# Optimization experiments

Hardware: AMD Instinct MI355X
Metric: run time of the kernel (lower is better)

Reference implementation:

```python
import jax, jax.numpy as jnp
import numpy as np

HEADS = 8
DIM_HEAD = 64
MAX_REL = 200  # max_rel_dist


def setup_inputs() -> dict:
    key = jax.random.key(0)
    ks = jax.random.split(key, 5)
    B, N, D = 4, 2048, 512
    x = jax.random.normal(ks[0], (B, N, D), dtype=jnp.float32)
    temporal_mask = jax.random.randint(ks[1], (N, N), 0, 2, dtype=jnp.int32)
    gamma = jnp.ones((D,), jnp.float32)
    beta = jnp.zeros((D,), jnp.float32)
    Wqkv = jax.random.normal(ks[2], (D, 3 * HEADS * DIM_HEAD), dtype=jnp.float32) * 0.02
    Wout = jax.random.normal(ks[3], (HEADS * DIM_HEAD, D), dtype=jnp.float32) * 0.02
    bout = jnp.zeros((D,), jnp.float32)
    rel_table = jax.random.normal(ks[4], (2 * MAX_REL - 1,), dtype=jnp.float32) * 0.02
    return {"x": x, "gamma": gamma, "beta": beta, "Wqkv": Wqkv, "Wout": Wout,
            "bout": bout, "rel_table": rel_table, "temporal_mask": temporal_mask}


def reference(x, gamma, beta, Wqkv, Wout, bout, rel_table, temporal_mask):
    B, N, D = x.shape
    scale = DIM_HEAD ** -0.5
    # LayerNorm
    mu = jnp.mean(x, axis=-1, keepdims=True)
    var = jnp.mean(jnp.square(x - mu), axis=-1, keepdims=True)
    xn = (x - mu) * jax.lax.rsqrt(var + 1e-5) * gamma + beta
    # QKV projection (no bias), split heads: b n (h d) -> b h n d
    qkv = xn @ Wqkv  # [B, N, 3*H*d]
    q, k, v = jnp.split(qkv, 3, axis=-1)
    split = lambda t: t.reshape(B, N, HEADS, DIM_HEAD).transpose(0, 2, 1, 3)
    q, k, v = split(q), split(k), split(v)
    # scores with learned relative-position bias
    dots = jnp.einsum('bhnd,bhmd->bhnm', q, k) * scale  # [B,H,N,N]
    idx = jnp.arange(N)
    rel = jnp.clip(idx[:, None] - idx[None, :], -(MAX_REL - 1), MAX_REL - 1) + MAX_REL - 1
    dots = dots + rel_table[rel][None, None, :, :]
    # temporal mask (0 -> -inf); large negative for grad safety
    dots = jnp.where(temporal_mask[None, None, :, :] == 0, jnp.float32(-1e9), dots)
    attn = jax.nn.softmax(dots, axis=-1)
    out = jnp.einsum('bhnm,bhmd->bhnd', attn, v)
    out = out.transpose(0, 2, 1, 3).reshape(B, N, HEADS * DIM_HEAD)
    return out @ Wout + bout
```

## Files before the change

kernel.cpp:

```cpp
#include <hip/hip_runtime.h>

typedef __attribute__((ext_vector_type(8))) short bf16x8;
typedef __attribute__((ext_vector_type(4))) short bf16x4;
typedef __attribute__((ext_vector_type(4))) float f32x4;
typedef unsigned short ushort_t;

#define B_ 4
#define H_ 8
#define N_ 2048
#define D_ 512
#define MAXREL 199
#define LOG2E 1.4426950408889634f

__device__ __forceinline__ ushort_t f2bf(float f) {
    union { float f; unsigned u; } v; v.f = f;
    unsigned r = v.u + 0x7fffu + ((v.u >> 16) & 1u);
    return (ushort_t)(r >> 16);
}
__device__ __forceinline__ float bf2f(ushort_t u) {
    union { unsigned u; float f; } v; v.u = ((unsigned)u) << 16;
    return v.f;
}
__device__ __forceinline__ float fexp2(float x) {
#if __has_builtin(__builtin_amdgcn_exp2f)
    return __builtin_amdgcn_exp2f(x);
#else
    return __expf(x * 0.6931471805599453f);
#endif
}
__device__ __forceinline__ unsigned cvt_pk_bf16(float lo, float hi) {
    unsigned r;
    asm("v_cvt_pk_bf16_f32 %0, %1, %2" : "=v"(r) : "v"(lo), "v"(hi));
    return r;
}
__device__ __forceinline__ void gl_lds16(const ushort_t* g, ushort_t* l) {
    __builtin_amdgcn_global_load_lds(
        (const __attribute__((address_space(1))) void*)g,
        (__attribute__((address_space(3))) void*)l,
        16, 0, 0);
}

#define PREP_BIAS  16384
#define PREP_LN    8192
#define PREP_WQ    768
#define PREP_WO    256
__global__ __launch_bounds__(256) void prep_kernel(const float* __restrict__ x,
                                                   const float* __restrict__ gamma,
                                                   const float* __restrict__ beta,
                                                   ushort_t* __restrict__ xn,
                                                   const float* __restrict__ Wqkv,
                                                   ushort_t* __restrict__ WqkvT,
                                                   const float* __restrict__ Wout,
                                                   ushort_t* __restrict__ WoutT,
                                                   const float* __restrict__ rel,
                                                   const int* __restrict__ mask,
                                                   ushort_t* __restrict__ bp) {
    __shared__ float smem[32 * 33];
    const int blk = blockIdx.x;
    const int t = threadIdx.x;

    if (blk < PREP_BIAS) {
        int idx = blk * 256 + t;
        int n = idx >> 11, m = idx & 2047;
        int dl = n - m;
        dl = dl < -MAXREL ? -MAXREL : (dl > MAXREL ? MAXREL : dl);
        float v = (mask[idx] == 0) ? -1e9f : rel[dl + MAXREL] * LOG2E;
        bp[idx] = f2bf(v);
    } else if (blk < PREP_BIAS + PREP_LN) {
        const int row = blk - PREP_BIAS;
        const float* xr = x + (size_t)row * D_;
        float v0 = xr[t];
        float v1 = xr[t + 256];
        float s = v0 + v1;
        for (int o = 32; o > 0; o >>= 1) s += __shfl_down(s, o);
        if ((t & 63) == 0) smem[t >> 6] = s;
        __syncthreads();
        float mu = (smem[0] + smem[1] + smem[2] + smem[3]) * (1.0f / D_);
        __syncthreads();
        float d0 = v0 - mu, d1 = v1 - mu;
        float s2 = d0 * d0 + d1 * d1;
        for (int o = 32; o > 0; o >>= 1) s2 += __shfl_down(s2, o);
        if ((t & 63) == 0) smem[t >> 6] = s2;
        __syncthreads();
        float var = (smem[0] + smem[1] + smem[2] + smem[3]) * (1.0f / D_);
        float rs = rsqrtf(var + 1e-5f);
        ushort_t* yr = xn + (size_t)row * D_;
        yr[t]       = f2bf(d0 * rs * gamma[t]       + beta[t]);
        yr[t + 256] = f2bf(d1 * rs * gamma[t + 256] + beta[t + 256]);
    } else {
        const float* W; ushort_t* Wt; int Nn, i;
        if (blk < PREP_BIAS + PREP_LN + PREP_WQ) {
            i = blk - (PREP_BIAS + PREP_LN); W = Wqkv; Wt = WqkvT; Nn = 1536;
        } else {
            i = blk - (PREP_BIAS + PREP_LN + PREP_WQ); W = Wout; Wt = WoutT; Nn = 512;
        }
        const int nb = Nn >> 5;
        const int bx = (i % nb) * 32, by = (i / nb) * 32;
        const int tx = t & 31, ty = t >> 5;
        float (*tile)[33] = (float(*)[33])smem;
        #pragma unroll
        for (int k = 0; k < 32; k += 8)
            tile[ty + k][tx] = W[(size_t)(by + ty + k) * Nn + bx + tx];
        __syncthreads();
        #pragma unroll
        for (int k = 0; k < 32; k += 8)
            Wt[(size_t)(bx + ty + k) * 512 + by + tx] = f2bf(tile[tx][ty + k]);
    }
}

__global__ __launch_bounds__(256) void gemm_qkv(const ushort_t* __restrict__ A,
                                                const ushort_t* __restrict__ Bt,
                                                ushort_t* __restrict__ qb,
                                                ushort_t* __restrict__ kb,
                                                ushort_t* __restrict__ vb) {
    __shared__ ushort_t As[128 * 32];
    __shared__ ushort_t Bs[128 * 32];
    const int t = threadIdx.x;
    const int lane = t & 63, w = t >> 6;
    const int m16 = lane & 15, quad = lane >> 4;
    const int wr = w >> 1, wc = w & 1;
    const int r0 = blockIdx.y * 128, c0 = blockIdx.x * 128;

    const ushort_t* Ag = A  + (size_t)(r0 + (t >> 2)) * D_ + (t & 3) * 8;
    const ushort_t* Bg = Bt + (size_t)(c0 + (t >> 2)) * D_ + (t & 3) * 8;
    ushort_t* AsW = As + w * 512;
    ushort_t* BsW = Bs + w * 512;

    f32x4 acc[4][4];
    #pragma unroll
    for (int i = 0; i < 4; i++)
        #pragma unroll
        for (int j = 0; j < 4; j++) acc[i][j] = (f32x4){0.f, 0.f, 0.f, 0.f};

    for (int k0 = 0; k0 < D_; k0 += 32) {
        gl_lds16(Ag + k0, AsW);
        gl_lds16(Ag + k0 + (size_t)64 * D_, AsW + 2048);
        gl_lds16(Bg + k0, BsW);
        gl_lds16(Bg + k0 + (size_t)64 * D_, BsW + 2048);
        __syncthreads();
        bf16x8 af[4], bfr[4];
        #pragma unroll
        for (int rt = 0; rt < 4; rt++)
            af[rt] = *(const bf16x8*)(As + (wr * 64 + rt * 16 + m16) * 32 + quad * 8);
        #pragma unroll
        for (int ct = 0; ct < 4; ct++)
            bfr[ct] = *(const bf16x8*)(Bs + (wc * 64 + ct * 16 + m16) * 32 + quad * 8);
        #pragma unroll
        for (int rt = 0; rt < 4; rt++)
            #pragma unroll
            for (int ct = 0; ct < 4; ct++)
                acc[rt][ct] = __builtin_amdgcn_mfma_f32_16x16x32_bf16(af[rt], bfr[ct], acc[rt][ct], 0, 0, 0);
        __syncthreads();
    }

    #pragma unroll
    for (int ct = 0; ct < 4; ct++) {
        int cc = c0 + wc * 64 + ct * 16;
        int which = cc >> 9;
        int h = (cc >> 6) & 7;
        int d = (cc & 63) + m16;
        #pragma unroll
        for (int rt = 0; rt < 4; rt++) {
            int rowb = r0 + wr * 64 + rt * 16 + quad * 4;
            int b = rowb >> 11, n0 = rowb & 2047;
            if (which == 0) {
                #pragma unroll
                for (int r = 0; r < 4; r++)
                    qb[((size_t)((b * H_ + h) * N_ + n0 + r)) * 64 + d] = f2bf(acc[rt][ct][r] * (0.125f * LOG2E));
            } else if (which == 1) {
                #pragma unroll
                for (int r = 0; r < 4; r++)
                    kb[((size_t)((b * H_ + h) * N_ + n0 + r)) * 64 + d] = f2bf(acc[rt][ct][r]);
            } else {
                union { ushort_t u4[4]; unsigned long long ll; } pk;
                #pragma unroll
                for (int r = 0; r < 4; r++) pk.u4[r] = f2bf(acc[rt][ct][r]);
                *(unsigned long long*)(vb + ((size_t)((b * H_ + h) * 64 + d)) * N_ + n0) = pk.ll;
            }
        }
    }
}

__global__ __launch_bounds__(256) void gemm_out(const ushort_t* __restrict__ A,
                                                const ushort_t* __restrict__ Bt,
                                                const float* __restrict__ bias,
                                                float* __restrict__ C) {
    __shared__ ushort_t As[64 * 32];
    __shared__ ushort_t Bs[128 * 32];
    const int t = threadIdx.x;
    const int lane = t & 63, w = t >> 6;
    const int m16 = lane & 15, quad = lane >> 4;
    const int wr = w >> 1, wc = w & 1;
    const int r0 = blockIdx.y * 64, c0 = blockIdx.x * 128;

    const ushort_t* Ag = A  + (size_t)(r0 + (t >> 2)) * D_ + (t & 3) * 8;
    const ushort_t* Bg = Bt + (size_t)(c0 + (t >> 2)) * D_ + (t & 3) * 8;
    ushort_t* AsW = As + w * 512;
    ushort_t* BsW = Bs + w * 512;

    f32x4 acc[2][4];
    #pragma unroll
    for (int i = 0; i < 2; i++)
        #pragma unroll
        for (int j = 0; j < 4; j++) acc[i][j] = (f32x4){0.f, 0.f, 0.f, 0.f};

    for (int k0 = 0; k0 < D_; k0 += 32) {
        gl_lds16(Ag + k0, AsW);
        gl_lds16(Bg + k0, BsW);
        gl_lds16(Bg + k0 + (size_t)64 * D_, BsW + 2048);
        __syncthreads();
        bf16x8 af[2], bfr[4];
        #pragma unroll
        for (int mf = 0; mf < 2; mf++)
            af[mf] = *(const bf16x8*)(As + (wr * 32 + mf * 16 + m16) * 32 + quad * 8);
        #pragma unroll
        for (int nt = 0; nt < 4; nt++)
            bfr[nt] = *(const bf16x8*)(Bs + (wc * 64 + nt * 16 + m16) * 32 + quad * 8);
        #pragma unroll
        for (int mf = 0; mf < 2; mf++)
            #pragma unroll
            for (int nt = 0; nt < 4; nt++)
                acc[mf][nt] = __builtin_amdgcn_mfma_f32_16x16x32_bf16(af[mf], bfr[nt], acc[mf][nt], 0, 0, 0);
        __syncthreads();
    }

    #pragma unroll
    for (int mf = 0; mf < 2; mf++) {
        #pragma unroll
        for (int nt = 0; nt < 4; nt++) {
            int col = c0 + wc * 64 + nt * 16 + m16;
            int row0 = r0 + wr * 32 + mf * 16 + quad * 4;
            float bv = bias[col];
            #pragma unroll
            for (int r = 0; r < 4; r++)
                C[(size_t)(row0 + r) * 512 + col] = acc[mf][nt][r] + bv;
        }
    }
}

__global__ __launch_bounds__(512, 4) void attn_mfma(const ushort_t* __restrict__ qb,
                                                    const ushort_t* __restrict__ kb,
                                                    const ushort_t* __restrict__ vb,
                                                    const ushort_t* __restrict__ bp,
                                                    ushort_t* __restrict__ attn) {
    __shared__ ushort_t Ks[2][64 * 64];
    __shared__ ushort_t Vs[2][64 * 64];

    const int t = threadIdx.x;
    const int w = t >> 6, lane = t & 63;
    const int m16 = lane & 15, quad = lane >> 4;
    const int id = blockIdx.x;
    const int bh = id & 31;
    const int qt = id >> 5;
    const int b = bh >> 3, h = bh & 7;
    const int n0w = qt * 128 + w * 16;

    const int srow = t >> 3, scb = t & 7;
    const int soff = srow * 64 + (scb ^ (srow & 7)) * 8;
    const ushort_t* kgbase = kb + ((size_t)bh * N_) * 64;
    const ushort_t* vgbase = vb + ((size_t)bh * 64) * N_;

    const ushort_t* qpb = qb + ((size_t)(bh * N_ + n0w + m16)) * 64 + quad * 8;
    bf16x8 qa0 = *(const bf16x8*)(qpb);
    bf16x8 qa1 = *(const bf16x8*)(qpb + 32);

    const ushort_t* bprow = bp + (size_t)(n0w + m16) * 2048 + quad * 4;

    const int srcA = m16 + 32 * (quad & 1);
    const int srcB = srcA + 16;
    const bool lowhalf = (quad < 2);

    *(bf16x8*)(&Ks[0][soff]) = *(const bf16x8*)(kgbase + (size_t)srow * 64 + scb * 8);
    *(bf16x8*)(&Vs[0][soff]) = *(const bf16x8*)(vgbase + (size_t)srow * N_ + scb * 8);
    __syncthreads();

    f32x4 o[4];
    #pragma unroll
    for (int nt = 0; nt < 4; nt++) o[nt] = (f32x4){0.f, 0.f, 0.f, 0.f};
    float rsum = 0.f;

    for (int jt = 0; jt < 32; jt++) {
        const int buf = jt & 1;
        const int j0 = jt * 64;
        const bool more = (jt < 31);

        bf16x8 kst, vst;
        if (more) {
            kst = *(const bf16x8*)(kgbase + (size_t)(j0 + 64 + srow) * 64 + scb * 8);
            vst = *(const bf16x8*)(vgbase + (size_t)srow * N_ + j0 + 64 + scb * 8);
        }

        bf16x4 bc[4];
        #pragma unroll
        for (int nt = 0; nt < 4; nt++) bc[nt] = *(const bf16x4*)(bprow + jt * 64 + nt * 16);

        unsigned pk[8];
        #pragma unroll
        for (int nt = 0; nt < 4; nt++) {
            f32x4 a2;
            #pragma unroll
            for (int r = 0; r < 4; r++) a2[r] = bf2f((ushort_t)bc[nt][r]);
            int kr = nt * 16 + m16;
            bf16x8 kf0 = *(const bf16x8*)(&Ks[buf][kr * 64 + ((quad) ^ (kr & 7)) * 8]);
            bf16x8 kf1 = *(const bf16x8*)(&Ks[buf][kr * 64 + ((quad + 4) ^ (kr & 7)) * 8]);
            a2 = __builtin_amdgcn_mfma_f32_16x16x32_bf16(kf0, qa0, a2, 0, 0, 0);
            a2 = __builtin_amdgcn_mfma_f32_16x16x32_bf16(kf1, qa1, a2, 0, 0, 0);
            float p0 = fexp2(a2[0]);
            float p1 = fexp2(a2[1]);
            float p2 = fexp2(a2[2]);
            float p3 = fexp2(a2[3]);
            rsum += (p0 + p1) + (p2 + p3);
            pk[nt * 2]     = cvt_pk_bf16(p0, p1);
            pk[nt * 2 + 1] = cvt_pk_bf16(p2, p3);
        }

        union { unsigned u[4]; bf16x8 v; } pa0u, pa1u;
        {
            unsigned e0 = __shfl(pk[0], srcA), o0 = __shfl(pk[2], srcA);
            unsigned e1 = __shfl(pk[1], srcA), o1 = __shfl(pk[3], srcA);
            unsigned e2 = __shfl(pk[0], srcB), o2 = __shfl(pk[2], srcB);
            unsigned e3 = __shfl(pk[1], srcB), o3 = __shfl(pk[3], srcB);
            pa0u.u[0] = lowhalf ? e0 : o0;
            pa0u.u[1] = lowhalf ? e1 : o1;
            pa0u.u[2] = lowhalf ? e2 : o2;
            pa0u.u[3] = lowhalf ? e3 : o3;
            unsigned f0 = __shfl(pk[4], srcA), g0 = __shfl(pk[6], srcA);
            unsigned f1 = __shfl(pk[5], srcA), g1 = __shfl(pk[7], srcA);
            unsigned f2 = __shfl(pk[4], srcB), g2 = __shfl(pk[6], srcB);
            unsigned f3 = __shfl(pk[5], srcB), g3 = __shfl(pk[7], srcB);
            pa1u.u[0] = lowhalf ? f0 : g0;
            pa1u.u[1] = lowhalf ? f1 : g1;
            pa1u.u[2] = lowhalf ? f2 : g2;
            pa1u.u[3] = lowhalf ? f3 : g3;
        }

        #pragma unroll
        for (int nt = 0; nt < 4; nt++) {
            int d = nt * 16 + m16;
            bf16x8 vf0 = *(const bf16x8*)(&Vs[buf][d * 64 + ((quad) ^ (d & 7)) * 8]);
            bf16x8 vf1 = *(const bf16x8*)(&Vs[buf][d * 64 + ((quad + 4) ^ (d & 7)) * 8]);
            o[nt] = __builtin_amdgcn_mfma_f32_16x16x32_bf16(pa0u.v, vf0, o[nt], 0, 0, 0);
            o[nt] = __builtin_amdgcn_mfma_f32_16x16x32_bf16(pa1u.v, vf1, o[nt], 0, 0, 0);
        }

        if (more) {
            *(bf16x8*)(&Ks[buf ^ 1][soff]) = kst;
            *(bf16x8*)(&Vs[buf ^ 1][soff]) = vst;
        }
        __syncthreads();
    }

    rsum += __shfl_xor(rsum, 16);
    rsum += __shfl_xor(rsum, 32);

    #pragma unroll
    for (int r = 0; r < 4; r++) {
        float inv = 1.0f / __shfl(rsum, quad * 4 + r);
        int n = n0w + quad * 4 + r;
        ushort_t* orow = attn + ((size_t)(b * N_ + n)) * 512 + h * 64 + m16;
        #pragma unroll
        for (int nt = 0; nt < 4; nt++) orow[nt * 16] = f2bf(o[nt][r] * inv);
    }
}

extern "C" void kernel_launch(void* const* d_in, const int* in_sizes, int n_in,
                              void* d_out, int out_size, void* d_ws, size_t ws_size,
                              hipStream_t stream) {
    const float* x     = (const float*)d_in[0];
    const float* gamma = (const float*)d_in[1];
    const float* beta  = (const float*)d_in[2];
    const float* Wqkv  = (const float*)d_in[3];
    const float* Wout  = (const float*)d_in[4];
    const float* bout  = (const float*)d_in[5];
    const float* rel   = (const float*)d_in[6];
    const int*   mask  = (const int*)d_in[7];
    float* out = (float*)d_out;

    char* wsb = (char*)d_ws;
    ushort_t* xn    = (ushort_t*)(wsb);
    ushort_t* attnb = (ushort_t*)(wsb + ( 8u << 20));
    ushort_t* qb    = (ushort_t*)(wsb + (16u << 20));
    ushort_t* kb    = (ushort_t*)(wsb + (24u << 20));
    ushort_t* vb    = (ushort_t*)(wsb + (32u << 20));
    ushort_t* WqkvT = (ushort_t*)(wsb + (40u << 20));
    ushort_t* WoutT = (ushort_t*)(wsb + (42u << 20));
    ushort_t* bp    = (ushort_t*)(wsb + (44u << 20));

    prep_kernel<<<PREP_BIAS + PREP_LN + PREP_WQ + PREP_WO, 256, 0, stream>>>(
        x, gamma, beta, xn, Wqkv, WqkvT, Wout, WoutT, rel, mask, bp);

    gemm_qkv<<<dim3(1536 / 128, 8192 / 128), 256, 0, stream>>>(xn, WqkvT, qb, kb, vb);

    attn_mfma<<<512, 512, 0, stream>>>(qb, kb, vb, bp, attnb);

    gemm_out<<<dim3(512 / 128, 8192 / 64), 256, 0, stream>>>(attnb, WoutT, bout, out);
}
```

Before: 210.6 us.

## Tile bias layout for contiguous loads and redistribute P via LDS instead of shuffles

The prep kernel now writes the combined bias/mask matrix in a tiled order matching the attention kernel's per-wave MFMA fragment layout, so each wave's bias loads per key tile become contiguous. The attention kernel also replaces the 16 cross-lane shuffles plus selects, used to rearrange the probability tile into MFMA A-operand layout, with a per-wave swizzled LDS write followed by two vector reads. This adds 16 KB of shared memory per block, which may reduce occupancy, and relies on in-wave ordering of LDS accesses without an explicit barrier.

After: 200.4 us. -4.8%, faster.

```diff
diff --git a/kernel.cpp b/kernel.cpp
--- a/kernel.cpp
+++ b/kernel.cpp
@@ -65,7 +65,9 @@
         int dl = n - m;
         dl = dl < -MAXREL ? -MAXREL : (dl > MAXREL ? MAXREL : dl);
         float v = (mask[idx] == 0) ? -1e9f : rel[dl + MAXREL] * LOG2E;
-        bp[idx] = f2bf(v);
+        int off = ((n >> 7) << 18) + ((m >> 6) << 13) + (((n >> 4) & 7) << 10)
+                + (((m >> 4) & 3) << 8) + (((m >> 2) & 3) << 6) + ((n & 15) << 2) + (m & 3);
+        bp[off] = f2bf(v);
     } else if (blk < PREP_BIAS + PREP_LN) {
         const int row = blk - PREP_BIAS;
         const float* xr = x + (size_t)row * D_;
@@ -245,6 +247,7 @@
                                                     ushort_t* __restrict__ attn) {
     __shared__ ushort_t Ks[2][64 * 64];
     __shared__ ushort_t Vs[2][64 * 64];
+    __shared__ ushort_t p_s[8][16 * 64];
 
     const int t = threadIdx.x;
     const int w = t >> 6, lane = t & 63;
@@ -264,11 +267,7 @@
     bf16x8 qa0 = *(const bf16x8*)(qpb);
     bf16x8 qa1 = *(const bf16x8*)(qpb + 32);
 
-    const ushort_t* bprow = bp + (size_t)(n0w + m16) * 2048 + quad * 4;
-
-    const int srcA = m16 + 32 * (quad & 1);
-    const int srcB = srcA + 16;
-    const bool lowhalf = (quad < 2);
+    const ushort_t* bpb = bp + ((size_t)qt << 18) + (w << 10) + (quad << 6) + (m16 << 2);
 
     *(bf16x8*)(&Ks[0][soff]) = *(const bf16x8*)(kgbase + (size_t)srow * 64 + scb * 8);
     *(bf16x8*)(&Vs[0][soff]) = *(const bf16x8*)(vgbase + (size_t)srow * N_ + scb * 8);
@@ -278,6 +277,8 @@
     #pragma unroll
     for (int nt = 0; nt < 4; nt++) o[nt] = (f32x4){0.f, 0.f, 0.f, 0.f};
     float rsum = 0.f;
+
+    ushort_t* pw = p_s[w];
 
     for (int jt = 0; jt < 32; jt++) {
         const int buf = jt & 1;
@@ -292,7 +293,7 @@
 
         bf16x4 bc[4];
         #pragma unroll
-        for (int nt = 0; nt < 4; nt++) bc[nt] = *(const bf16x4*)(bprow + jt * 64 + nt * 16);
+        for (int nt = 0; nt < 4; nt++) bc[nt] = *(const bf16x4*)(bpb + (jt << 13) + (nt << 8));
 
         unsigned pk[8];
         #pragma unroll
@@ -314,33 +315,23 @@
             pk[nt * 2 + 1] = cvt_pk_bf16(p2, p3);
         }
 
-        union { unsigned u[4]; bf16x8 v; } pa0u, pa1u;
-        {
-            unsigned e0 = __shfl(pk[0], srcA), o0 = __shfl(pk[2], srcA);
-            unsigned e1 = __shfl(pk[1], srcA), o1 = __shfl(pk[3], srcA);
-            unsigned e2 = __shfl(pk[0], srcB), o2 = __shfl(pk[2], srcB);
-            unsigned e3 = __shfl(pk[1], srcB), o3 = __shfl(pk[3], srcB);
-            pa0u.u[0] = lowhalf ? e0 : o0;
-            pa0u.u[1] = lowhalf ? e1 : o1;
-            pa0u.u[2] = lowhalf ? e2 : o2;
-            pa0u.u[3] = lowhalf ? e3 : o3;
-            unsigned f0 = __shfl(pk[4], srcA), g0 = __shfl(pk[6], srcA);
-            unsigned f1 = __shfl(pk[5], srcA), g1 = __shfl(pk[7], srcA);
-            unsigned f2 = __shfl(pk[4], srcB), g2 = __shfl(pk[6], srcB);
-            unsigned f3 = __shfl(pk[5], srcB), g3 = __shfl(pk[7], srcB);
-            pa1u.u[0] = lowhalf ? f0 : g0;
-            pa1u.u[1] = lowhalf ? f1 : g1;
-            pa1u.u[2] = lowhalf ? f2 : g2;
-            pa1u.u[3] = lowhalf ? f3 : g3;
-        }
+        #pragma unroll
+        for (int j = 0; j < 8; j++) {
+            int chunk = 2 * (j >> 1) + (quad >> 1);
+            int pos = (quad & 1) * 4 + 2 * (j & 1);
+            *(unsigned*)(pw + m16 * 64 + ((chunk ^ (m16 & 7)) << 3) + pos) = pk[j];
+        }
+
+        bf16x8 pa0 = *(const bf16x8*)(pw + m16 * 64 + ((quad ^ (m16 & 7)) << 3));
+        bf16x8 pa1 = *(const bf16x8*)(pw + m16 * 64 + (((quad + 4) ^ (m16 & 7)) << 3));
 
         #pragma unroll
         for (int nt = 0; nt < 4; nt++) {
             int d = nt * 16 + m16;
             bf16x8 vf0 = *(const bf16x8*)(&Vs[buf][d * 64 + ((quad) ^ (d & 7)) * 8]);
             bf16x8 vf1 = *(const bf16x8*)(&Vs[buf][d * 64 + ((quad + 4) ^ (d & 7)) * 8]);
-            o[nt] = __builtin_amdgcn_mfma_f32_16x16x32_bf16(pa0u.v, vf0, o[nt], 0, 0, 0);
-            o[nt] = __builtin_amdgcn_mfma_f32_16x16x32_bf16(pa1u.v, vf1, o[nt], 0, 0, 0);
+            o[nt] = __builtin_amdgcn_mfma_f32_16x16x32_bf16(pa0, vf0, o[nt], 0, 0, 0);
+            o[nt] = __builtin_amdgcn_mfma_f32_16x16x32_bf16(pa1, vf1, o[nt], 0, 0, 0);
         }
 
         if (more) {
```
